# Kernel tuning notes

Measured on AMD Instinct MI355X. Metric: run time of the kernel, lower is better.

Reference implementation:

```python
import jax, jax.numpy as jnp
import numpy as np

N_GROUPS = 32
EPS = 1e-6


def group_norm(x, gamma, beta):
    # x: (b, c, h, w); 32 groups, eps=1e-6, affine
    b, c, h, w = x.shape
    xg = x.reshape(b, N_GROUPS, c // N_GROUPS, h, w)
    mean = xg.mean(axis=(2, 3, 4), keepdims=True)
    var = xg.var(axis=(2, 3, 4), keepdims=True)
    xg = (xg - mean) * jax.lax.rsqrt(var + EPS)
    x = xg.reshape(b, c, h, w)
    return x * gamma[None, :, None, None] + beta[None, :, None, None]


def setup_inputs() -> dict:
    key = jax.random.key(0)
    ks = jax.random.split(key, 8)
    b, c, h, w = 4, 512, 64, 64
    sc = 1.0 / np.sqrt(c)
    return {
        "x": jax.random.normal(ks[0], (b, c, h, w), jnp.float32),
        "gn_w": jnp.ones((c,), jnp.float32),
        "gn_b": jnp.zeros((c,), jnp.float32),
        "wq": jax.random.normal(ks[1], (c, c), jnp.float32) * sc,
        "bq": jnp.zeros((c,), jnp.float32),
        "wk": jax.random.normal(ks[2], (c, c), jnp.float32) * sc,
        "bk": jnp.zeros((c,), jnp.float32),
        "wv": jax.random.normal(ks[3], (c, c), jnp.float32) * sc,
        "bv": jnp.zeros((c,), jnp.float32),
        "wo": jax.random.normal(ks[4], (c, c), jnp.float32) * sc,
        "bo": jnp.zeros((c,), jnp.float32),
    }


def reference(x, gn_w, gn_b, wq, bq, wk, bk, wv, bv, wo, bo):
    b, c, h, w = x.shape
    s = c ** (-0.5)
    xn = group_norm(x, gn_w, gn_b)
    xf = xn.reshape(b, c, h * w)  # (b, c, hw)
    # 1x1 convs == channel matmuls: weight (out_c, in_c)
    q = jnp.einsum('oc,bci->boi', wq, xf) + bq[None, :, None]
    k = jnp.einsum('oc,bci->boi', wk, xf) + bk[None, :, None]
    v = jnp.einsum('oc,bci->boi', wv, xf) + bv[None, :, None]
    attn = jnp.einsum('bci,bcj->bij', q, k) * s  # (b, hw, hw)
    attn = jax.nn.softmax(attn, axis=-1)
    out = jnp.einsum('bij,bcj->bci', attn, v)  # (b, c, hw)
    out = jnp.einsum('oc,bci->boi', wo, out) + bo[None, :, None]
    return out.reshape(b, c, h, w) + x
```

## Files before the change

### kernel.cpp

```cpp
#include <hip/hip_runtime.h>

#define B 4
#define C 512
#define HW 4096
#define NG 32
#define GSZ 65536
#define KROW 528

typedef unsigned short u16;
typedef unsigned int u32;
typedef __attribute__((ext_vector_type(8))) short short8;
typedef __attribute__((ext_vector_type(4))) float f32x4;

__device__ __forceinline__ float bf2f(u16 u) {
    union { u32 i; float f; } x; x.i = ((u32)u) << 16; return x.f;
}
__device__ __forceinline__ u16 f2bf(float f) {
    union { u32 i; float f; } x; x.f = f;
    u32 r = x.i + 0x7FFF + ((x.i >> 16) & 1);
    return (u16)(r >> 16);
}
__device__ __forceinline__ u32 cvtpk(float lo, float hi) {
    u32 r;
    asm("v_cvt_pk_bf16_f32 %0, %1, %2" : "=v"(r) : "v"(lo), "v"(hi));
    return r;
}

__device__ __forceinline__ void gld16(const u16* g, u16* l) {
    __builtin_amdgcn_global_load_lds(
        (const __attribute__((address_space(1))) void*)g,
        (__attribute__((address_space(3))) void*)l, 16, 0, 0);
}

__global__ __launch_bounds__(256) void conv_kernel(
        const float* __restrict__ wq, const float* __restrict__ wk,
        const float* __restrict__ wv, const float* __restrict__ wo,
        u16* __restrict__ dst) {
    const int mat = blockIdx.y;
    const float* src = (mat == 0) ? wq : (mat == 1) ? wk : (mat == 2) ? wv : wo;
    const int idx = (blockIdx.x * 256 + threadIdx.x) * 4;
    float4 v = *(const float4*)(src + idx);
    uint2 r = make_uint2(cvtpk(v.x, v.y), cvtpk(v.z, v.w));
    *(uint2*)(dst + (size_t)mat * (C * C) + idx) = r;
}

__global__ __launch_bounds__(256) void gn_stats_kernel(
        const float* __restrict__ x, float2* __restrict__ part) {
    const int gl = blockIdx.x;
    const int qt = blockIdx.y;
    const size_t base = (size_t)gl * GSZ + (size_t)qt * (GSZ / 4);
    const int tid = threadIdx.x;
    float s = 0.f, s2 = 0.f;
    for (int i = tid * 4; i < GSZ / 4; i += 1024) {
        float4 v4 = *(const float4*)(x + base + i);
        s  += v4.x + v4.y + v4.z + v4.w;
        s2 += v4.x*v4.x + v4.y*v4.y + v4.z*v4.z + v4.w*v4.w;
    }
    #pragma unroll
    for (int off = 32; off > 0; off >>= 1) {
        s  += __shfl_down(s, off, 64);
        s2 += __shfl_down(s2, off, 64);
    }
    __shared__ float rs[4], rs2[4];
    int lane = tid & 63, wid = tid >> 6;
    if (lane == 0) { rs[wid] = s; rs2[wid] = s2; }
    __syncthreads();
    if (tid == 0) {
        part[gl * 4 + qt] = make_float2(rs[0] + rs[1] + rs[2] + rs[3],
                                        rs2[0] + rs2[1] + rs2[2] + rs2[3]);
    }
}

__global__ __launch_bounds__(256) void gn_apply_kernel(
        const float* __restrict__ x, const float* __restrict__ gamma,
        const float* __restrict__ beta, const float2* __restrict__ part,
        u16* __restrict__ xnT) {
    const int b = blockIdx.y;
    const int i0 = blockIdx.x * 32;
    const int tid = threadIdx.x;
    __shared__ float gm[512], bt[512];
    __shared__ __align__(16) u16 tile[32 * 512];

    for (int c = tid; c < 512; c += 256) {
        int g = c >> 4;
        const float2* pp = part + ((size_t)b * 32 + g) * 4;
        float2 p0 = pp[0], p1 = pp[1], p2 = pp[2], p3 = pp[3];
        float mean = (p0.x + p1.x + p2.x + p3.x) * (1.f / GSZ);
        float var  = (p0.y + p1.y + p2.y + p3.y) * (1.f / GSZ) - mean * mean;
        float rstd = rsqrtf(var + 1e-6f);
        float gg = gamma[c] * rstd;
        gm[c] = gg;
        bt[c] = beta[c] - mean * gg;
    }
    __syncthreads();
    const int ci = tid >> 5;
    const int ii = tid & 31;
    const float* xb = x + (size_t)b * 512 * 4096 + i0;
    #pragma unroll 4
    for (int p = 0; p < 64; p++) {
        int c = p * 8 + ci;
        float v = xb[(size_t)c * 4096 + ii] * gm[c] + bt[c];
        tile[ii * 512 + (c ^ ((ii & 7) << 3))] = f2bf(v);
    }
    __syncthreads();
    u16* dst = xnT + ((size_t)b * HW + i0) * C;
    #pragma unroll
    for (int p = 0; p < 8; p++) {
        int i = p * 4 + (tid >> 6);
        int ch = tid & 63;
        *(uint4*)(dst + (size_t)i * C + ch * 8) =
            *(const uint4*)&tile[i * 512 + ((ch ^ (i & 7)) << 3)];
    }
}

__global__ __launch_bounds__(256) void qkv_kernel(
        const u16* __restrict__ xnT, const u16* __restrict__ wb,
        const float* __restrict__ bq, const float* __restrict__ bk,
        const float* __restrict__ bv,
        u16* __restrict__ qT, u16* __restrict__ kT, u16* __restrict__ vimg) {
    const int mat = blockIdx.y >> 2;
    const int oT0 = (blockIdx.y & 3) * 128;
    const int iT0 = blockIdx.x * 128;
    const int b = blockIdx.z;
    const u16* Ag = xnT + ((size_t)b * HW + iT0) * C;
    const u16* Bg = wb + (size_t)mat * C * C + (size_t)oT0 * C;
    const float* bias = (mat == 0) ? bq : (mat == 1) ? bk : bv;

    const int tid = threadIdx.x;
    const int w = tid >> 6, lane = tid & 63;
    const int qd = lane >> 4, nn = lane & 15;
    const int wm = w & 1, wn = w >> 1;

    __shared__ __align__(16) u16 smem[16384];
    u16* As0 = smem;
    u16* Bs0 = smem + 8192;

    f32x4 acc[4][4];
    #pragma unroll
    for (int mt = 0; mt < 4; mt++)
        #pragma unroll
        for (int nt = 0; nt < 4; nt++) acc[mt][nt] = (f32x4){0.f, 0.f, 0.f, 0.f};

    auto stage = [&](u16* dst, const u16* g, int c0) {
        #pragma unroll
        for (int p = 0; p < 2; p++) {
            int rbase = 32 * w + 16 * p;
            int row = rbase + (lane >> 2);
            gld16(g + (size_t)row * C + c0 + (((lane & 3) ^ ((row >> 1) & 3)) << 3),
                  dst + rbase * 32);
        }
    };

    stage(As0, Ag, 0);
    stage(Bs0, Bg, 0);

    for (int kt = 0; kt < 16; kt++) {
        const int cur = kt & 1;
        __syncthreads();
        if (kt < 15) {
            stage(As0 + (cur ^ 1) * 4096, Ag, (kt + 1) * 32);
            stage(Bs0 + (cur ^ 1) * 4096, Bg, (kt + 1) * 32);
        }
        const u16* Ac = As0 + cur * 4096;
        const u16* Bc = Bs0 + cur * 4096;
        short8 af[4], bf[4];
        #pragma unroll
        for (int mt = 0; mt < 4; mt++) {
            int row = 64 * wm + 16 * mt + nn;
            af[mt] = *(const short8*)&Ac[row * 32 + ((qd ^ ((row >> 1) & 3)) << 3)];
        }
        #pragma unroll
        for (int nt = 0; nt < 4; nt++) {
            int row = 64 * wn + 16 * nt + nn;
            bf[nt] = *(const short8*)&Bc[row * 32 + ((qd ^ ((row >> 1) & 3)) << 3)];
        }
        #pragma unroll
        for (int mt = 0; mt < 4; mt++)
            #pragma unroll
            for (int nt = 0; nt < 4; nt++)
                acc[mt][nt] = __builtin_amdgcn_mfma_f32_16x16x32_bf16(af[mt], bf[nt], acc[mt][nt], 0, 0, 0);
    }

    __syncthreads();
    u16* dt = smem;

    if (mat < 2) {
        #pragma unroll
        for (int nt = 0; nt < 4; nt++) {
            int o_l = 64 * wn + 16 * nt + nn;
            float bb = bias[oT0 + o_l];
            #pragma unroll
            for (int mt = 0; mt < 4; mt++) {
                int i_l = 64 * wm + 16 * mt + qd * 4;
                dt[(i_l + 0) * 128 + o_l] = f2bf(acc[mt][nt][0] + bb);
                dt[(i_l + 1) * 128 + o_l] = f2bf(acc[mt][nt][1] + bb);
                dt[(i_l + 2) * 128 + o_l] = f2bf(acc[mt][nt][2] + bb);
                dt[(i_l + 3) * 128 + o_l] = f2bf(acc[mt][nt][3] + bb);
            }
        }
        __syncthreads();
        u16* dstT = ((mat == 0) ? qT : kT) + ((size_t)b * HW + iT0) * C + oT0;
        #pragma unroll
        for (int p = 0; p < 8; p++) {
            int i_l = p * 16 + (tid >> 4);
            int ch = tid & 15;
            *(uint4*)(dstT + (size_t)i_l * C + ch * 8) = *(const uint4*)&dt[i_l * 128 + ch * 8];
        }
    } else {
        #pragma unroll
        for (int nt = 0; nt < 4; nt++) {
            int c_l = 64 * wn + 16 * nt + nn;
            float bb = bias[oT0 + c_l];
            #pragma unroll
            for (int mt = 0; mt < 4; mt++) {
                int i_l = 64 * wm + 16 * mt + qd * 4;
                int lc = i_l >> 5;
                int j0 = i_l & 31;
                union { uint2 u; ushort4 s; } st;
                st.u = make_uint2(cvtpk(acc[mt][nt][0] + bb, acc[mt][nt][1] + bb),
                                  cvtpk(acc[mt][nt][2] + bb, acc[mt][nt][3] + bb));
                *(ushort4*)&dt[lc * 4096 + c_l * 32 +
                               (((j0 >> 3) ^ ((c_l >> 2) & 3)) << 3) + (j0 & 7)] = st.s;
            }
        }
        __syncthreads();
        u16* vb = vimg + (size_t)b * 128 * 16384;
        const int chb = iT0 >> 5;
        #pragma unroll
        for (int p = 0; p < 8; p++) {
            int lc = p >> 1, half = p & 1;
            *(uint4*)(vb + (size_t)(chb + lc) * 16384 + oT0 * 32 + half * 2048 + tid * 8) =
                *(const uint4*)&dt[lc * 4096 + half * 2048 + tid * 8];
        }
    }
}

__global__ __launch_bounds__(256, 2) void attn_kernel(
        const u16* __restrict__ qT, const u16* __restrict__ kT,
        const u16* __restrict__ vimg, u16* __restrict__ oT) {
    const int b = blockIdx.y;
    const int i0 = blockIdx.x * 32;
    const int tid = threadIdx.x;
    const int w = tid >> 6;
    const int lane = tid & 63;
    const int q = lane >> 4;
    const int n = lane & 15;
    const int rw = w & 1;
    const int jh = w >> 1;

    __shared__ __align__(16) u16 kbuf[2][32 * KROW];
    __shared__ __align__(16) u16 pbuf[2][32 * 40];
    __shared__ __align__(16) float mflag[2][4];
    __shared__ __align__(16) float lpart[2][32];

    short8 qf[16];
    {
        const u16* qrow = qT + ((size_t)b * HW + i0 + rw * 16 + n) * C + q * 8;
        #pragma unroll
        for (int k = 0; k < 16; k++) {
            uint4 u = *(const uint4*)(qrow + k * 32);
            qf[k] = *(const short8*)&u;
        }
    }
    f32x4 oacc[2][8];
    #pragma unroll
    for (int mt = 0; mt < 2; mt++)
        #pragma unroll
        for (int nt = 0; nt < 8; nt++)
            oacc[mt][nt] = (f32x4){0.f, 0.f, 0.f, 0.f};
    float mreg = 0.f;
    float lsum[4] = {0.f, 0.f, 0.f, 0.f};

    const u16* kTb = kT + (size_t)b * HW * C;
    const u16* vTb = vimg + (size_t)b * 128 * 16384;

    auto stageK = [&](int gc, int buf) {
        const u16* gk = kTb + (size_t)gc * 32 * C;
        #pragma unroll
        for (int ii = 0; ii < 8; ii++) {
            int j = w * 8 + ii;
            gld16(gk + (size_t)j * C + ((lane ^ (j & 7)) << 3), &kbuf[buf][j * KROW]);
        }
    };

    const float scale = 0.04419417382415922f;
    stageK(0, 0);
    stageK(1, 1);
    __syncthreads();

    auto s_phase = [&](int slot, int par, float alpha) {
        f32x4 s0 = {0.f,0.f,0.f,0.f}, s1 = {0.f,0.f,0.f,0.f};
        f32x4 s2 = {0.f,0.f,0.f,0.f}, s3 = {0.f,0.f,0.f,0.f};
        const int sw = n & 7;
        const u16* kb = kbuf[slot] + (jh * 16 + n) * KROW;
        __builtin_amdgcn_s_setprio(1);
        #pragma unroll
        for (int m = 0; m < 4; m++) {
            short8 b0 = *(const short8*)&kb[(((4 * m + 0) * 4 + q) ^ sw) << 3];
            short8 b1 = *(const short8*)&kb[(((4 * m + 1) * 4 + q) ^ sw) << 3];
            short8 b2 = *(const short8*)&kb[(((4 * m + 2) * 4 + q) ^ sw) << 3];
            short8 b3 = *(const short8*)&kb[(((4 * m + 3) * 4 + q) ^ sw) << 3];
            s0 = __builtin_amdgcn_mfma_f32_16x16x32_bf16(qf[4 * m + 0], b0, s0, 0, 0, 0);
            s1 = __builtin_amdgcn_mfma_f32_16x16x32_bf16(qf[4 * m + 1], b1, s1, 0, 0, 0);
            s2 = __builtin_amdgcn_mfma_f32_16x16x32_bf16(qf[4 * m + 2], b2, s2, 0, 0, 0);
            s3 = __builtin_amdgcn_mfma_f32_16x16x32_bf16(qf[4 * m + 3], b3, s3, 0, 0, 0);
        }
        __builtin_amdgcn_s_setprio(0);
        float sv[4];
        #pragma unroll
        for (int r = 0; r < 4; r++) sv[r] = ((s0[r] + s1[r]) + (s2[r] + s3[r])) * scale;
        float pm = fmaxf(fmaxf(sv[0], sv[1]), fmaxf(sv[2], sv[3]));
        float flagv = -1e30f;
        if (__any(pm > mreg + 8.0f)) {
            float mx = pm;
            mx = fmaxf(mx, __shfl_xor(mx, 1));
            mx = fmaxf(mx, __shfl_xor(mx, 2));
            mx = fmaxf(mx, __shfl_xor(mx, 4));
            mx = fmaxf(mx, __shfl_xor(mx, 8));
            mx = fmaxf(mx, __shfl_xor(mx, 16));
            mx = fmaxf(mx, __shfl_xor(mx, 32));
            flagv = mx;
        }
        if (lane == 0) mflag[par][w] = flagv;
        float p0 = __expf(sv[0] - mreg), p1 = __expf(sv[1] - mreg);
        float p2 = __expf(sv[2] - mreg), p3 = __expf(sv[3] - mreg);
        lsum[0] = lsum[0] * alpha + p0;
        lsum[1] = lsum[1] * alpha + p1;
        lsum[2] = lsum[2] * alpha + p2;
        lsum[3] = lsum[3] * alpha + p3;
        u32 a = cvtpk(p0, p1), c = cvtpk(p2, p3);
        u16* pb = &pbuf[par][(rw * 16 + q * 4) * 40 + jh * 16 + n];
        pb[0]      = (u16)a;
        pb[40]     = (u16)(a >> 16);
        pb[80]     = (u16)c;
        pb[120]    = (u16)(c >> 16);
    };

    s_phase(0, 0, 1.f);
    __syncthreads();

    #pragma unroll 1
    for (int t = 0; t < 128; ++t) {
        const int cur = t & 1;
        f32x4 fl = *(const f32x4*)mflag[cur];
        short8 pf[2];
        #pragma unroll
        for (int mt = 0; mt < 2; mt++)
            pf[mt] = *(const short8*)&pbuf[cur][(mt * 16 + n) * 40 + q * 8];
        uint4 vpf[8];
        {
            const u16* gv = vTb + (size_t)t * 16384;
            #pragma unroll
            for (int nt = 0; nt < 8; nt++) {
                int c = w * 128 + nt * 16 + n;
                vpf[nt] = *(const uint4*)&gv[c * 32 + ((q ^ ((c >> 2) & 3)) << 3)];
            }
        }
        if (t < 126) stageK(t + 2, cur);
        float mnew = fmaxf(fmaxf(mreg, fl[0]), fmaxf(fmaxf(fl[1], fl[2]), fl[3]));
        float alpha = 1.f;
        if (mnew > mreg) { alpha = __expf(mreg - mnew); mreg = mnew; }
        if (t < 127) {
            s_phase(cur ^ 1, cur ^ 1, alpha);
        } else {
            #pragma unroll
            for (int r = 0; r < 4; r++) lsum[r] *= alpha;
        }
        __builtin_amdgcn_s_setprio(1);
        #pragma unroll
        for (int nt = 0; nt < 8; nt++) {
            short8 vf = *(const short8*)&vpf[nt];
            #pragma unroll
            for (int mt = 0; mt < 2; mt++)
                oacc[mt][nt] = __builtin_amdgcn_mfma_f32_16x16x32_bf16(pf[mt], vf, oacc[mt][nt], 0, 0, 0);
        }
        __builtin_amdgcn_s_setprio(0);
        if (alpha != 1.f) {
            #pragma unroll
            for (int mt = 0; mt < 2; mt++)
                #pragma unroll
                for (int nt = 0; nt < 8; nt++) {
                    oacc[mt][nt][0] *= alpha; oacc[mt][nt][1] *= alpha;
                    oacc[mt][nt][2] *= alpha; oacc[mt][nt][3] *= alpha;
                }
        }
        __syncthreads();
    }
    #pragma unroll
    for (int r = 0; r < 4; r++) {
        float l = lsum[r];
        l += __shfl_xor(l, 1);
        l += __shfl_xor(l, 2);
        l += __shfl_xor(l, 4);
        l += __shfl_xor(l, 8);
        if (n == 0) lpart[jh][rw * 16 + q * 4 + r] = l;
    }
    __syncthreads();
    #pragma unroll
    for (int mt = 0; mt < 2; mt++) {
        float inv[4];
        #pragma unroll
        for (int r = 0; r < 4; r++) {
            int row = mt * 16 + q * 4 + r;
            inv[r] = 1.f / (lpart[0][row] + lpart[1][row]);
        }
        #pragma unroll
        for (int nt = 0; nt < 8; nt++) {
            int cc = w * 128 + nt * 16 + n;
            size_t base = ((size_t)b * HW + i0 + mt * 16 + q * 4) * C + cc;
            oT[base        ] = f2bf(oacc[mt][nt][0] * inv[0]);
            oT[base +   C  ] = f2bf(oacc[mt][nt][1] * inv[1]);
            oT[base + 2 * C] = f2bf(oacc[mt][nt][2] * inv[2]);
            oT[base + 3 * C] = f2bf(oacc[mt][nt][3] * inv[3]);
        }
    }
}

__global__ __launch_bounds__(256) void proj_kernel(
        const u16* __restrict__ oT, const u16* __restrict__ wob,
        const float* __restrict__ bo, const float* __restrict__ x,
        float* __restrict__ out) {
    const int o0 = blockIdx.y * 128;
    const int i0t = blockIdx.x * 128;
    const int b = blockIdx.z;
    const u16* Ag = wob + (size_t)o0 * C;
    const u16* Bg = oT + ((size_t)b * HW + i0t) * C;

    const int tid = threadIdx.x;
    const int w = tid >> 6, lane = tid & 63;
    const int qd = lane >> 4, nn = lane & 15;
    const int wm = w & 1, wn = w >> 1;

    __shared__ __align__(16) u16 As[2][128 * 32];
    __shared__ __align__(16) u16 Bs[2][128 * 32];

    f32x4 acc[4][4];
    #pragma unroll
    for (int mt = 0; mt < 4; mt++)
        #pragma unroll
        for (int nt = 0; nt < 4; nt++) acc[mt][nt] = (f32x4){0.f, 0.f, 0.f, 0.f};

    auto stage = [&](u16* dst, const u16* g, int c0) {
        #pragma unroll
        for (int p = 0; p < 2; p++) {
            int rbase = 32 * w + 16 * p;
            int row = rbase + (lane >> 2);
            gld16(g + (size_t)row * C + c0 + (((lane & 3) ^ ((row >> 1) & 3)) << 3),
                  dst + rbase * 32);
        }
    };

    stage(As[0], Ag, 0);
    stage(Bs[0], Bg, 0);

    for (int kt = 0; kt < 16; kt++) {
        const int cur = kt & 1;
        __syncthreads();
        if (kt < 15) {
            stage(As[cur ^ 1], Ag, (kt + 1) * 32);
            stage(Bs[cur ^ 1], Bg, (kt + 1) * 32);
        }
        short8 af[4], bf[4];
        #pragma unroll
        for (int mt = 0; mt < 4; mt++) {
            int row = 64 * wm + 16 * mt + nn;
            af[mt] = *(const short8*)&As[cur][row * 32 + ((qd ^ ((row >> 1) & 3)) << 3)];
        }
        #pragma unroll
        for (int nt = 0; nt < 4; nt++) {
            int row = 64 * wn + 16 * nt + nn;
            bf[nt] = *(const short8*)&Bs[cur][row * 32 + ((qd ^ ((row >> 1) & 3)) << 3)];
        }
        #pragma unroll
        for (int mt = 0; mt < 4; mt++)
            #pragma unroll
            for (int nt = 0; nt < 4; nt++)
                acc[mt][nt] = __builtin_amdgcn_mfma_f32_16x16x32_bf16(af[mt], bf[nt], acc[mt][nt], 0, 0, 0);
    }

    #pragma unroll
    for (int mt = 0; mt < 4; mt++) {
        #pragma unroll
        for (int r = 0; r < 4; r++) {
            int o = o0 + 64 * wm + 16 * mt + qd * 4 + r;
            float bb = bo[o];
            #pragma unroll
            for (int nt = 0; nt < 4; nt++) {
                int i = i0t + 64 * wn + 16 * nt + nn;
                size_t idx = ((size_t)b * C + o) * HW + i;
                out[idx] = acc[mt][nt][r] + bb + x[idx];
            }
        }
    }
}

extern "C" void kernel_launch(void* const* d_in, const int* in_sizes, int n_in,
                              void* d_out, int out_size, void* d_ws, size_t ws_size,
                              hipStream_t stream) {
    const float* x    = (const float*)d_in[0];
    const float* gn_w = (const float*)d_in[1];
    const float* gn_b = (const float*)d_in[2];
    const float* wq   = (const float*)d_in[3];
    const float* bq   = (const float*)d_in[4];
    const float* wk   = (const float*)d_in[5];
    const float* bk   = (const float*)d_in[6];
    const float* wv   = (const float*)d_in[7];
    const float* bv   = (const float*)d_in[8];
    const float* wo   = (const float*)d_in[9];
    const float* bo   = (const float*)d_in[10];
    float* out = (float*)d_out;

    const size_t WSZ = (size_t)C * C;
    const size_t S1  = (size_t)B * C * HW;
    u16* wb    = (u16*)d_ws;
    u16* wob   = wb + 3 * WSZ;
    u16* xnT   = wob + WSZ;
    u16* qT    = xnT + S1;
    u16* kT    = qT + S1;
    u16* vimg  = kT + S1;
    u16* oT    = vimg + S1;
    float2* part = (float2*)(oT + S1);

    hipLaunchKernelGGL(conv_kernel,     dim3(256, 4), dim3(256), 0, stream, wq, wk, wv, wo, wb);
    hipLaunchKernelGGL(gn_stats_kernel, dim3(B*NG, 4), dim3(256), 0, stream, x, part);
    hipLaunchKernelGGL(gn_apply_kernel, dim3(HW/32, B), dim3(256), 0, stream,
                       x, gn_w, gn_b, part, xnT);
    hipLaunchKernelGGL(qkv_kernel,      dim3(HW/128, 12, B), dim3(256), 0, stream,
                       xnT, wb, bq, bk, bv, qT, kT, vimg);
    hipLaunchKernelGGL(attn_kernel,     dim3(HW/32, B), dim3(256), 0, stream,
                       qT, kT, vimg, oT);
    hipLaunchKernelGGL(proj_kernel,     dim3(HW/128, C/128, B), dim3(256), 0, stream, oT, wob, bo, x, out);
}
```

Measured before the change: 386.1 us.

## Double attention query tile to 64 rows with 512-thread blocks

The attention kernel now processes 64 query rows per block with 8 waves instead of 32 rows with 4 waves. Each staged K tile and each V tile load is shared by twice as many queries, cutting global and LDS traffic per query. Each wave now covers 64 channels by 64 rows in place of 128 by 32, and the launch grid is halved. The risk is register pressure: __launch_bounds__(512, 2) tightens the per-thread register budget while the resident Q fragments and accumulators stay the same size, so spills or lower occupancy are possible.

```diff
diff --git a/kernel.cpp b/kernel.cpp
--- a/kernel.cpp
+++ b/kernel.cpp
@@ -235,23 +235,23 @@
     }
 }
 
-__global__ __launch_bounds__(256, 2) void attn_kernel(
+__global__ __launch_bounds__(512, 2) void attn_kernel(
         const u16* __restrict__ qT, const u16* __restrict__ kT,
         const u16* __restrict__ vimg, u16* __restrict__ oT) {
     const int b = blockIdx.y;
-    const int i0 = blockIdx.x * 32;
+    const int i0 = blockIdx.x * 64;
     const int tid = threadIdx.x;
     const int w = tid >> 6;
     const int lane = tid & 63;
     const int q = lane >> 4;
     const int n = lane & 15;
-    const int rw = w & 1;
-    const int jh = w >> 1;
+    const int rw = w & 3;
+    const int jh = w >> 2;
 
     __shared__ __align__(16) u16 kbuf[2][32 * KROW];
-    __shared__ __align__(16) u16 pbuf[2][32 * 40];
-    __shared__ __align__(16) float mflag[2][4];
-    __shared__ __align__(16) float lpart[2][32];
+    __shared__ __align__(16) u16 pbuf[2][64 * 40];
+    __shared__ __align__(16) float mflag[2][8];
+    __shared__ __align__(16) float lpart[2][64];
 
     short8 qf[16];
     {
@@ -262,12 +262,12 @@
             qf[k] = *(const short8*)&u;
         }
     }
-    f32x4 oacc[2][8];
-    #pragma unroll
-    for (int mt = 0; mt < 2; mt++)
-        #pragma unroll
-        for (int nt = 0; nt < 8; nt++)
-            oacc[mt][nt] = (f32x4){0.f, 0.f, 0.f, 0.f};
+    f32x4 oacc[4][4];
+    #pragma unroll
+    for (int mt = 0; mt < 4; mt++)
+        #pragma unroll
+        for (int ct = 0; ct < 4; ct++)
+            oacc[mt][ct] = (f32x4){0.f, 0.f, 0.f, 0.f};
     float mreg = 0.f;
     float lsum[4] = {0.f, 0.f, 0.f, 0.f};
 
@@ -277,8 +277,8 @@
     auto stageK = [&](int gc, int buf) {
         const u16* gk = kTb + (size_t)gc * 32 * C;
         #pragma unroll
-        for (int ii = 0; ii < 8; ii++) {
-            int j = w * 8 + ii;
+        for (int ii = 0; ii < 4; ii++) {
+            int j = w * 4 + ii;
             gld16(gk + (size_t)j * C + ((lane ^ (j & 7)) << 3), &kbuf[buf][j * KROW]);
         }
     };
@@ -342,22 +342,25 @@
     #pragma unroll 1
     for (int t = 0; t < 128; ++t) {
         const int cur = t & 1;
-        f32x4 fl = *(const f32x4*)mflag[cur];
-        short8 pf[2];
-        #pragma unroll
-        for (int mt = 0; mt < 2; mt++)
+        f32x4 fl0 = *(const f32x4*)&mflag[cur][0];
+        f32x4 fl1 = *(const f32x4*)&mflag[cur][4];
+        short8 pf[4];
+        #pragma unroll
+        for (int mt = 0; mt < 4; mt++)
             pf[mt] = *(const short8*)&pbuf[cur][(mt * 16 + n) * 40 + q * 8];
-        uint4 vpf[8];
+        uint4 vpf[4];
         {
             const u16* gv = vTb + (size_t)t * 16384;
             #pragma unroll
-            for (int nt = 0; nt < 8; nt++) {
-                int c = w * 128 + nt * 16 + n;
-                vpf[nt] = *(const uint4*)&gv[c * 32 + ((q ^ ((c >> 2) & 3)) << 3)];
+            for (int ct = 0; ct < 4; ct++) {
+                int c = w * 64 + ct * 16 + n;
+                vpf[ct] = *(const uint4*)&gv[c * 32 + ((q ^ ((c >> 2) & 3)) << 3)];
             }
         }
         if (t < 126) stageK(t + 2, cur);
-        float mnew = fmaxf(fmaxf(mreg, fl[0]), fmaxf(fmaxf(fl[1], fl[2]), fl[3]));
+        float mnew = mreg;
+        #pragma unroll
+        for (int i = 0; i < 4; i++) mnew = fmaxf(mnew, fmaxf(fl0[i], fl1[i]));
         float alpha = 1.f;
         if (mnew > mreg) { alpha = __expf(mreg - mnew); mreg = mnew; }
         if (t < 127) {
@@ -368,20 +371,20 @@
         }
         __builtin_amdgcn_s_setprio(1);
         #pragma unroll
-        for (int nt = 0; nt < 8; nt++) {
-            short8 vf = *(const short8*)&vpf[nt];
-            #pragma unroll
-            for (int mt = 0; mt < 2; mt++)
-                oacc[mt][nt] = __builtin_amdgcn_mfma_f32_16x16x32_bf16(pf[mt], vf, oacc[mt][nt], 0, 0, 0);
+        for (int ct = 0; ct < 4; ct++) {
+            short8 vf = *(const short8*)&vpf[ct];
+            #pragma unroll
+            for (int mt = 0; mt < 4; mt++)
+                oacc[mt][ct] = __builtin_amdgcn_mfma_f32_16x16x32_bf16(pf[mt], vf, oacc[mt][ct], 0, 0, 0);
         }
         __builtin_amdgcn_s_setprio(0);
         if (alpha != 1.f) {
             #pragma unroll
-            for (int mt = 0; mt < 2; mt++)
+            for (int mt = 0; mt < 4; mt++)
                 #pragma unroll
-                for (int nt = 0; nt < 8; nt++) {
-                    oacc[mt][nt][0] *= alpha; oacc[mt][nt][1] *= alpha;
-                    oacc[mt][nt][2] *= alpha; oacc[mt][nt][3] *= alpha;
+                for (int ct = 0; ct < 4; ct++) {
+                    oacc[mt][ct][0] *= alpha; oacc[mt][ct][1] *= alpha;
+                    oacc[mt][ct][2] *= alpha; oacc[mt][ct][3] *= alpha;
                 }
         }
         __syncthreads();
@@ -397,7 +400,7 @@
     }
     __syncthreads();
     #pragma unroll
-    for (int mt = 0; mt < 2; mt++) {
+    for (int mt = 0; mt < 4; mt++) {
         float inv[4];
         #pragma unroll
         for (int r = 0; r < 4; r++) {
@@ -405,13 +408,13 @@
             inv[r] = 1.f / (lpart[0][row] + lpart[1][row]);
         }
         #pragma unroll
-        for (int nt = 0; nt < 8; nt++) {
-            int cc = w * 128 + nt * 16 + n;
+        for (int ct = 0; ct < 4; ct++) {
+            int cc = w * 64 + ct * 16 + n;
             size_t base = ((size_t)b * HW + i0 + mt * 16 + q * 4) * C + cc;
-            oT[base        ] = f2bf(oacc[mt][nt][0] * inv[0]);
-            oT[base +   C  ] = f2bf(oacc[mt][nt][1] * inv[1]);
-            oT[base + 2 * C] = f2bf(oacc[mt][nt][2] * inv[2]);
-            oT[base + 3 * C] = f2bf(oacc[mt][nt][3] * inv[3]);
+            oT[base        ] = f2bf(oacc[mt][ct][0] * inv[0]);
+            oT[base +   C  ] = f2bf(oacc[mt][ct][1] * inv[1]);
+            oT[base + 2 * C] = f2bf(oacc[mt][ct][2] * inv[2]);
+            oT[base + 3 * C] = f2bf(oacc[mt][ct][3] * inv[3]);
         }
     }
 }
@@ -527,7 +530,7 @@
                        x, gn_w, gn_b, part, xnT);
     hipLaunchKernelGGL(qkv_kernel,      dim3(HW/128, 12, B), dim3(256), 0, stream,
                        xnT, wb, bq, bk, bv, qT, kT, vimg);
-    hipLaunchKernelGGL(attn_kernel,     dim3(HW/32, B), dim3(256), 0, stream,
+    hipLaunchKernelGGL(attn_kernel,     dim3(HW/64, B), dim3(512), 0, stream,
                        qT, kT, vimg, oT);
     hipLaunchKernelGGL(proj_kernel,     dim3(HW/128, C/128, B), dim3(256), 0, stream, oT, wob, bo, x, out);
 }
```

After: 366.0 us. 1.05x faster.
